# Kernel tuning notes

Measured on AMD Instinct MI355X. Metric: run time of the kernel, lower is better.

## Reference

```python
import jax, jax.numpy as jnp
import numpy as np

N, P, C, S, H, CLS = 32, 16, 256, 128, 4, 3000
DH = C // H
EPS = 1e-5


def setup_inputs() -> dict:
    key = jax.random.key(0)
    ks = jax.random.split(key, 8)
    sh = (N, P, C, S)
    return {
        "t_f": jax.random.normal(ks[0], sh, jnp.float32),
        "t_s": jax.random.normal(ks[1], sh, jnp.float32),
        "t_l": jax.random.normal(ks[2], sh, jnp.float32),
        # grouped 1x1 conv weights, one [out_ch, in_ch] matrix per part
        "decay_w": jax.random.normal(ks[3], (P, C, 3 * C), jnp.float32) * 0.02,
        "qkv_w": jax.random.normal(ks[4], (P, 3 * C, C), jnp.float32) * 0.02,
        "out_w": jax.random.normal(ks[5], (P, C, C), jnp.float32) * 0.02,
        # per-part BatchNorm1d affine params
        "gamma": jnp.ones((P, C), jnp.float32),
        "beta": jnp.zeros((P, C), jnp.float32),
        # classifier fc: [in_planes, class_num] (broadcast over parts)
        "fc": jax.random.normal(ks[6], (C, CLS), jnp.float32) * 0.02,
    }


def reference(t_f, t_s, t_l, decay_w, qkv_w, out_w, gamma, beta, fc):
    n, p, c, s = t_f.shape
    h, dh = H, DH
    scale = dh ** -0.5

    # decay_c: grouped 1x1 conv, 3c -> c per part
    x_cat = jnp.concatenate([t_f, t_s, t_l], axis=2)            # [n,p,3c,s]
    t_all = jnp.einsum('npis,poi->npos', x_cat, decay_w)        # [n,p,c,s]

    # Attention.to_qkv: grouped 1x1 conv, c -> 3c per part
    qkv = jnp.einsum('npcs,pqc->npqs', t_all, qkv_w)            # [n,p,3c,s]
    qkv = qkv.reshape(n, p, 3, h, dh, s).transpose(2, 0, 3, 1, 4, 5)  # [3,n,h,p,dh,s]
    q, k, v = qkv[0], qkv[1], qkv[2]

    # frame-frame attention per (head, part): [n,h,p,s,s]
    dots = jnp.einsum('nhpcs,nhpct->nhpst', q, k) * scale
    attn = jax.nn.softmax(dots, axis=-1)

    o = jnp.einsum('nhpst,nhpct->nhpcs', attn, v)               # [n,h,p,dh,s]
    o = o.transpose(0, 2, 1, 3, 4).reshape(n, p, c, s)          # [n,p,c,s]
    o = jnp.einsum('npcs,poc->npos', o, out_w)                  # to_out grouped conv

    # residual + max over frames
    wpv = (o + t_all).max(axis=-1)                              # [n,p,c]

    # select_topk_part (topk_num == 1 forced by squeeze(2) in torch code):
    # argmax over frames of column-summed attention, gather that frame of t_f, sum heads
    idx = jnp.argmax(attn.sum(axis=-2), axis=-1)                # [n,h,p]
    ib = jnp.broadcast_to(idx[:, :, :, None, None], (n, h, p, c, 1))
    sel = jnp.take_along_axis(t_f[:, None], ib, axis=-1)[..., 0]  # [n,h,p,c]
    sel = sel.sum(axis=1)                                       # [n,p,c]

    # per-part BatchNorm1d in training mode (batch statistics over n)
    mean = wpv.mean(axis=0)                                     # [p,c]
    var = wpv.var(axis=0)                                       # biased, as torch BN
    pf = (wpv - mean) / jnp.sqrt(var + EPS) * gamma + beta      # [n,p,c]

    cls = jnp.einsum('npc,ck->npk', pf, fc)                     # [n,p,class_num]
    return cls, wpv.transpose(1, 0, 2), sel.transpose(1, 0, 2)
```

## Files before the change

### kernel.cpp

```cpp
#include <hip/hip_runtime.h>
#include <math.h>

#define N_ 32
#define P_ 16
#define C_ 256
#define S_ 128
#define H_ 4
#define CLS_ 3000

typedef __attribute__((ext_vector_type(4))) float f4v;
typedef __attribute__((ext_vector_type(4))) float f32x4;
typedef __attribute__((ext_vector_type(8))) short short8;
typedef __attribute__((ext_vector_type(4))) unsigned short us4;

__device__ __forceinline__ unsigned short f2bf(float x){
    unsigned u = __float_as_uint(x);
    u += 0x7fffu + ((u >> 16) & 1u);
    return (unsigned short)(u >> 16);
}
__device__ __forceinline__ float bf2f(unsigned short h){
    return __uint_as_float(((unsigned)h) << 16);
}

typedef __attribute__((address_space(1))) const unsigned int gu32_t;
typedef __attribute__((address_space(3))) unsigned int lu32_t;
__device__ __forceinline__ void gload16(const void* g, void* l){
    __builtin_amdgcn_global_load_lds((gu32_t*)g, (lu32_t*)l, 16, 0, 0);
}

__global__ void wsplit(const float* __restrict__ dw, const float* __restrict__ qw,
                       const float* __restrict__ ow,
                       unsigned short* __restrict__ wdh, unsigned short* __restrict__ wdl,
                       unsigned short* __restrict__ wqh, unsigned short* __restrict__ wql,
                       unsigned short* __restrict__ woh){
    int i = blockIdx.x * 256 + threadIdx.x;
    int stride = gridDim.x * 256;
    for (; i < 3145728; i += stride){
        float a = dw[i]; unsigned short h = f2bf(a);
        wdh[i] = h; wdl[i] = f2bf(a - bf2f(h));
        float b = qw[i]; unsigned short h2 = f2bf(b);
        wqh[i] = h2; wql[i] = f2bf(b - bf2f(h2));
        if (i < 1048576) woh[i] = f2bf(ow[i]);
    }
}

__global__ __launch_bounds__(256) void fct_kernel(const float* __restrict__ fc,
                                                  unsigned short* __restrict__ fcT){
    int n = blockIdx.x * 256 + threadIdx.x;
    if (n < CLS_){
        for (int c = 0; c < 256; ++c) fcT[(size_t)n * 256 + c] = f2bf(fc[(size_t)c * CLS_ + n]);
    } else {
        for (int c = 0; c < 256; ++c) fcT[(size_t)n * 256 + c] = 0;
    }
}

__global__ __launch_bounds__(256) void gemm0t(
    const float* __restrict__ t_f, const float* __restrict__ t_s,
    const float* __restrict__ t_l,
    const unsigned short* __restrict__ Whi, const unsigned short* __restrict__ Wlo,
    unsigned short* __restrict__ outH, unsigned short* __restrict__ outL,
    int n0, int cnp)
{
    __shared__ unsigned short sm[24576];
    float* Tf = (float*)sm;
    unsigned short* AhL = sm + 8192;
    unsigned short* AlL = sm + 12288;
    unsigned short* BhL = sm + 16384;
    unsigned short* BlL = sm + 20480;
    unsigned short* Ep  = sm;

    const int id = blockIdx.x;
    const int xcd = id & 7;
    const int r = id >> 3;
    const int ppl = r / (cnp * 2);
    const int rr = r % (cnp * 2);
    const int n_l = rr >> 1;
    const int o_t = rr & 1;
    const int p = xcd * 2 + ppl;
    const int np_l = n_l * 16 + p;
    const int o0 = o_t * 128;
    const size_t np_g = (size_t)(n0 + n_l) * 16 + p;

    const int tid = threadIdx.x;
    const int w = tid >> 6, l = tid & 63;
    const int lr = l & 15, lg = l >> 4;
    const int ws0 = (w & 1) * 64, wo0 = (w >> 1) * 64;
    const int s2 = tid & 127, khalf = tid >> 7;

    const unsigned short* Wp_h = Whi + ((size_t)p * 256 + o0) * 768;
    const unsigned short* Wp_l = Wlo + ((size_t)p * 256 + o0) * 768;

    f32x4 acc[4][4];
#pragma unroll
    for (int i = 0; i < 4; ++i)
#pragma unroll
        for (int j = 0; j < 4; ++j) acc[i][j] = (f32x4){0.f, 0.f, 0.f, 0.f};

    for (int k0 = 0; k0 < 768; k0 += 32){
        const int t = k0 >> 8;
        const float* src = (t == 0) ? t_f : ((t == 1) ? t_s : t_l);
        const float* xbase = src + (np_g * 256 + (k0 & 255)) * 128;
#pragma unroll
        for (int it = 0; it < 4; ++it){
            int lin = (w * 4 + it) * 64 + l;
            gload16(xbase + lin * 4, Tf + lin * 4);
        }
#pragma unroll
        for (int it = 0; it < 2; ++it){
            int lin = (w * 2 + it) * 64 + l;
            int row = lin >> 2, ch = lin & 3;
            int sk = ((ch ^ ((row >> 1) & 3)) << 3);
            gload16(Wp_h + (size_t)row * 768 + k0 + sk, BhL + lin * 8);
            gload16(Wp_l + (size_t)row * 768 + k0 + sk, BlL + lin * 8);
        }
        __syncthreads();
        {
            short8 h0, h1, l0, l1;
#pragma unroll
            for (int j = 0; j < 8; ++j){
                float v = Tf[(khalf * 16 + j) * 128 + s2];
                unsigned short hh = f2bf(v);
                h0[j] = (short)hh; l0[j] = (short)f2bf(v - bf2f(hh));
            }
#pragma unroll
            for (int j = 0; j < 8; ++j){
                float v = Tf[(khalf * 16 + 8 + j) * 128 + s2];
                unsigned short hh = f2bf(v);
                h1[j] = (short)hh; l1[j] = (short)f2bf(v - bf2f(hh));
            }
            int sb = (s2 >> 1) & 3;
            int c0 = (khalf * 2) ^ sb, c1 = (khalf * 2 + 1) ^ sb;
            *(short8*)(AhL + s2 * 32 + c0 * 8) = h0;
            *(short8*)(AhL + s2 * 32 + c1 * 8) = h1;
            *(short8*)(AlL + s2 * 32 + c0 * 8) = l0;
            *(short8*)(AlL + s2 * 32 + c1 * 8) = l1;
        }
        __syncthreads();
        short8 ah[4], al[4];
#pragma unroll
        for (int sf = 0; sf < 4; ++sf){
            int row = ws0 + sf * 16 + lr;
            int cof = (lg ^ ((row >> 1) & 3)) << 3;
            ah[sf] = *(const short8*)(AhL + row * 32 + cof);
            al[sf] = *(const short8*)(AlL + row * 32 + cof);
        }
#pragma unroll
        for (int of = 0; of < 4; ++of){
            int row = wo0 + of * 16 + lr;
            int cof = (lg ^ ((row >> 1) & 3)) << 3;
            short8 bh = *(const short8*)(BhL + row * 32 + cof);
            short8 bl = *(const short8*)(BlL + row * 32 + cof);
#pragma unroll
            for (int sf = 0; sf < 4; ++sf){
                acc[sf][of] = __builtin_amdgcn_mfma_f32_16x16x32_bf16(ah[sf], bh, acc[sf][of], 0, 0, 0);
                acc[sf][of] = __builtin_amdgcn_mfma_f32_16x16x32_bf16(ah[sf], bl, acc[sf][of], 0, 0, 0);
                acc[sf][of] = __builtin_amdgcn_mfma_f32_16x16x32_bf16(al[sf], bh, acc[sf][of], 0, 0, 0);
            }
        }
        __syncthreads();
    }

#pragma unroll
    for (int plane = 0; plane < 2; ++plane){
#pragma unroll
        for (int sf = 0; sf < 4; ++sf)
#pragma unroll
            for (int of = 0; of < 4; ++of){
                int col = wo0 + of * 16 + lr;
#pragma unroll
                for (int r2 = 0; r2 < 4; ++r2){
                    int row = ws0 + sf * 16 + lg * 4 + r2;
                    float v = acc[sf][of][r2];
                    unsigned short hh = f2bf(v);
                    unsigned short q = plane ? f2bf(v - bf2f(hh)) : hh;
                    Ep[row * 136 + col] = q;
                }
            }
        __syncthreads();
        unsigned short* dst = plane ? outL : outH;
#pragma unroll
        for (int it = 0; it < 8; ++it){
            int idx = tid + 256 * it;
            int row = idx >> 4, seg = (idx & 15) * 8;
            *(short8*)(dst + (size_t)np_l * 128 * 256 + (size_t)row * 256 + o0 + seg) =
                *(const short8*)(Ep + row * 136 + seg);
        }
        __syncthreads();
    }
}

template<int KEXT, int APITCH, int ND, int MODE, int OPITCH, int TOB>
__global__ __launch_bounds__(256) void gemm3(
    const unsigned short* __restrict__ Ah_g, const unsigned short* __restrict__ Al_g,
    const unsigned short* __restrict__ Whi, const unsigned short* __restrict__ Wlo,
    const unsigned short* __restrict__ resH, const unsigned short* __restrict__ resL,
    unsigned short* __restrict__ outH, unsigned short* __restrict__ outL,
    float* __restrict__ outF, int n0, int cnp)
{
    constexpr int T3 = (MODE == 2) ? 0 : 1;
    constexpr int OB = ND / TOB;
    constexpr int OF = TOB / 32;
    __shared__ unsigned short sm[T3 ? 17408 : (4096 + TOB * 32)];
    unsigned short* AhL = sm;
    unsigned short* BhL = sm + 4096;
    unsigned short* AlL = T3 ? (sm + 8192) : sm;
    unsigned short* BlL = T3 ? (sm + 12288) : sm;
    unsigned short* Ep = sm;
    __shared__ float cmax[2][2][64];

    const int id = blockIdx.x;
    const int xcd = id & 7;
    const int r = id >> 3;
    const int ppl = r / (cnp * OB);
    const int rr = r % (cnp * OB);
    const int n_l = rr / OB;
    const int o_t = rr % OB;
    const int p = xcd * 2 + ppl;
    const int np_l = n_l * 16 + p;
    const int o0 = o_t * TOB;

    const int tid = threadIdx.x;
    const int w = tid >> 6, l = tid & 63;
    const int lr = l & 15, lg = l >> 4;
    const int ws0 = (w & 1) * 64, wo0 = (w >> 1) * (TOB / 2);
    const size_t aBase = (size_t)np_l * 128 * APITCH;
    const unsigned short* Wp_h = Whi + ((size_t)p * ND + o0) * KEXT;
    const unsigned short* Wp_l = T3 ? (Wlo + ((size_t)p * ND + o0) * KEXT) : Wp_h;

    f32x4 acc[4][OF];
#pragma unroll
    for (int i = 0; i < 4; ++i)
#pragma unroll
        for (int j = 0; j < OF; ++j) acc[i][j] = (f32x4){0.f, 0.f, 0.f, 0.f};

    for (int k0 = 0; k0 < KEXT; k0 += 32){
#pragma unroll
        for (int it = 0; it < 2; ++it){
            int slot = w * 2 + it;
            int lin = slot * 64 + l;
            int row = lin >> 2, ch = lin & 3;
            int sk = ((ch ^ ((row >> 1) & 3)) << 3);
            gload16(Ah_g + aBase + (size_t)row * APITCH + k0 + sk, AhL + slot * 512);
            if (T3)
                gload16(Al_g + aBase + (size_t)row * APITCH + k0 + sk, AlL + slot * 512);
        }
#pragma unroll
        for (int it = 0; it < TOB / 64; ++it){
            int slot = w * (TOB / 64) + it;
            int lin = slot * 64 + l;
            int row = lin >> 2, ch = lin & 3;
            int sk = ((ch ^ ((row >> 1) & 3)) << 3);
            gload16(Wp_h + (size_t)row * KEXT + k0 + sk, BhL + slot * 512);
            if (T3)
                gload16(Wp_l + (size_t)row * KEXT + k0 + sk, BlL + slot * 512);
        }
        __syncthreads();
        short8 ah[4], al[4];
#pragma unroll
        for (int sf = 0; sf < 4; ++sf){
            int row = ws0 + sf * 16 + lr;
            int cof = (lg ^ ((row >> 1) & 3)) << 3;
            ah[sf] = *(const short8*)(AhL + row * 32 + cof);
            if (T3) al[sf] = *(const short8*)(AlL + row * 32 + cof);
        }
#pragma unroll
        for (int of = 0; of < OF; ++of){
            int row = wo0 + of * 16 + lr;
            int cof = (lg ^ ((row >> 1) & 3)) << 3;
            short8 bh = *(const short8*)(BhL + row * 32 + cof);
            short8 bl = bh;
            if (T3) bl = *(const short8*)(BlL + row * 32 + cof);
#pragma unroll
            for (int sf = 0; sf < 4; ++sf){
                acc[sf][of] = __builtin_amdgcn_mfma_f32_16x16x32_bf16(ah[sf], bh, acc[sf][of], 0, 0, 0);
                if (T3){
                    acc[sf][of] = __builtin_amdgcn_mfma_f32_16x16x32_bf16(ah[sf], bl, acc[sf][of], 0, 0, 0);
                    acc[sf][of] = __builtin_amdgcn_mfma_f32_16x16x32_bf16(al[sf], bh, acc[sf][of], 0, 0, 0);
                }
            }
        }
        __syncthreads();
    }

    if (MODE != 2){
#pragma unroll
        for (int plane = 0; plane < 2; ++plane){
#pragma unroll
            for (int sf = 0; sf < 4; ++sf)
#pragma unroll
                for (int of = 0; of < OF; ++of){
                    int col = wo0 + of * 16 + lr;
#pragma unroll
                    for (int r2 = 0; r2 < 4; ++r2){
                        int row = ws0 + sf * 16 + lg * 4 + r2;
                        float v = acc[sf][of][r2];
                        unsigned short hh = f2bf(v);
                        unsigned short q = plane ? f2bf(v - bf2f(hh)) : hh;
                        Ep[row * 136 + col] = q;
                    }
                }
            __syncthreads();
            unsigned short* dst = plane ? outL : outH;
#pragma unroll
            for (int it = 0; it < 8; ++it){
                int idx = tid + 256 * it;
                int row = idx >> 4, seg = (idx & 15) * 8;
                *(short8*)(dst + (size_t)np_l * 128 * OPITCH + (size_t)row * OPITCH + o0 + seg) =
                    *(const short8*)(Ep + row * 136 + seg);
            }
            __syncthreads();
        }
    } else {
        const int n_g = n0 + n_l;
#pragma unroll
        for (int of = 0; of < OF; ++of){
            int oc = o0 + wo0 + of * 16 + lr;
            float m = -INFINITY;
#pragma unroll
            for (int sf = 0; sf < 4; ++sf){
#pragma unroll
                for (int r2 = 0; r2 < 4; ++r2){
                    int s = ws0 + sf * 16 + lg * 4 + r2;
                    size_t ri = (size_t)np_l * 128 * 256 + (size_t)s * 256 + oc;
                    float v = acc[sf][of][r2] + bf2f(resH[ri]) + bf2f(resL[ri]);
                    m = fmaxf(m, v);
                }
            }
            m = fmaxf(m, __shfl_xor(m, 16));
            m = fmaxf(m, __shfl_xor(m, 32));
            if (l < 16) cmax[w >> 1][w & 1][of * 16 + l] = m;
        }
        __syncthreads();
        if (tid < TOB){
            int oh = tid >> 5, col = tid & 31;
            float v = fmaxf(cmax[oh][0][col], cmax[oh][1][col]);
            outF[((size_t)p * N_ + n_g) * C_ + o0 + oh * 32 + col] = v;
        }
    }
}

__global__ __launch_bounds__(256) void attn3(unsigned short* __restrict__ qH,
                                             const unsigned short* __restrict__ qL,
                                             int* __restrict__ idxA, int n0, int cnp){
    __shared__ char smraw[17408 + 34816 + 2048];
    unsigned short* Vs = (unsigned short*)smraw;
    unsigned short* Pm = (unsigned short*)(smraw + 17408);
    float* csW = (float*)(smraw + 17408 + 34816);
    unsigned short* Ot = (unsigned short*)smraw;

    const int id = blockIdx.x;
    const int xcd = id & 7;
    const int r = id >> 3;
    const int ppl = r / (cnp * 4);
    const int rr = r % (cnp * 4);
    const int n_l = rr >> 2, h = rr & 3;
    const int p = xcd * 2 + ppl;
    const int np_l = n_l * 16 + p;
    const int tid = threadIdx.x, w = tid >> 6, l = tid & 63;
    const int lr = l & 15, lg = l >> 4;
    unsigned short* baseH = qH + (size_t)np_l * 128 * 768;
    const unsigned short* baseL = qL + (size_t)np_l * 128 * 768;

#pragma unroll
    for (int it = 0; it < 8; ++it){
        int idx = tid + 256 * it;
        int t = idx >> 4, d4 = (idx & 15) * 4;
        us4 v = *(const us4*)(baseH + (size_t)t * 768 + 512 + h * 64 + d4);
#pragma unroll
        for (int j = 0; j < 4; ++j) Vs[(d4 + j) * 136 + t] = v[j];
    }

    short8 qh[2][2], ql[2][2];
#pragma unroll
    for (int sf = 0; sf < 2; ++sf)
#pragma unroll
        for (int ks = 0; ks < 2; ++ks){
            size_t off = (size_t)(w * 32 + sf * 16 + lr) * 768 + h * 64 + ks * 32 + lg * 8;
            qh[sf][ks] = *(const short8*)(baseH + off);
            ql[sf][ks] = *(const short8*)(baseL + off);
        }

    f32x4 dacc[2][8];
#pragma unroll
    for (int i = 0; i < 2; ++i)
#pragma unroll
        for (int j = 0; j < 8; ++j) dacc[i][j] = (f32x4){0.f, 0.f, 0.f, 0.f};

#pragma unroll
    for (int tf = 0; tf < 8; ++tf){
#pragma unroll
        for (int ks = 0; ks < 2; ++ks){
            size_t off = (size_t)(tf * 16 + lr) * 768 + 256 + h * 64 + ks * 32 + lg * 8;
            short8 kh = *(const short8*)(baseH + off);
            short8 kl = *(const short8*)(baseL + off);
#pragma unroll
            for (int sf = 0; sf < 2; ++sf){
                dacc[sf][tf] = __builtin_amdgcn_mfma_f32_16x16x32_bf16(qh[sf][ks], kh, dacc[sf][tf], 0, 0, 0);
                dacc[sf][tf] = __builtin_amdgcn_mfma_f32_16x16x32_bf16(qh[sf][ks], kl, dacc[sf][tf], 0, 0, 0);
                dacc[sf][tf] = __builtin_amdgcn_mfma_f32_16x16x32_bf16(ql[sf][ks], kh, dacc[sf][tf], 0, 0, 0);
            }
        }
    }

    float csp[8];
#pragma unroll
    for (int tf = 0; tf < 8; ++tf) csp[tf] = 0.f;
#pragma unroll
    for (int sf = 0; sf < 2; ++sf){
#pragma unroll
        for (int r2 = 0; r2 < 4; ++r2){
            float m = -INFINITY;
#pragma unroll
            for (int tf = 0; tf < 8; ++tf) m = fmaxf(m, dacc[sf][tf][r2]);
            m = fmaxf(m, __shfl_xor(m, 1)); m = fmaxf(m, __shfl_xor(m, 2));
            m = fmaxf(m, __shfl_xor(m, 4)); m = fmaxf(m, __shfl_xor(m, 8));
            float e[8]; float sum = 0.f;
#pragma unroll
            for (int tf = 0; tf < 8; ++tf){
                e[tf] = __expf(0.125f * (dacc[sf][tf][r2] - m)); sum += e[tf];
            }
            sum += __shfl_xor(sum, 1); sum += __shfl_xor(sum, 2);
            sum += __shfl_xor(sum, 4); sum += __shfl_xor(sum, 8);
            float inv = 1.f / sum;
            int s = w * 32 + sf * 16 + lg * 4 + r2;
#pragma unroll
            for (int tf = 0; tf < 8; ++tf){
                float pv = e[tf] * inv;
                Pm[s * 136 + tf * 16 + lr] = f2bf(pv);
                csp[tf] += pv;
            }
        }
    }
#pragma unroll
    for (int tf = 0; tf < 8; ++tf){
        float v = csp[tf];
        v += __shfl_xor(v, 16); v += __shfl_xor(v, 32);
        if (l < 16) csW[w * 128 + tf * 16 + l] = v;
    }
    __syncthreads();

    f32x4 oacc[8];
#pragma unroll
    for (int i = 0; i < 8; ++i) oacc[i] = (f32x4){0.f, 0.f, 0.f, 0.f};
#pragma unroll
    for (int ks = 0; ks < 4; ++ks){
        short8 av = *(const short8*)(Vs + (w * 16 + lr) * 136 + ks * 32 + lg * 8);
#pragma unroll
        for (int sf = 0; sf < 8; ++sf){
            short8 bp = *(const short8*)(Pm + (sf * 16 + lr) * 136 + ks * 32 + lg * 8);
            oacc[sf] = __builtin_amdgcn_mfma_f32_16x16x32_bf16(av, bp, oacc[sf], 0, 0, 0);
        }
    }
    __syncthreads();

    if (tid < 64){
        float v0 = csW[tid] + csW[128 + tid] + csW[256 + tid] + csW[384 + tid];
        float v1 = csW[64 + tid] + csW[192 + tid] + csW[320 + tid] + csW[448 + tid];
        float bv; int bi;
        if (v1 > v0){ bv = v1; bi = 64 + tid; } else { bv = v0; bi = tid; }
#pragma unroll
        for (int msk = 1; msk <= 32; msk <<= 1){
            float ov = __shfl_xor(bv, msk); int oi = __shfl_xor(bi, msk);
            if (ov > bv || (ov == bv && oi < bi)){ bv = ov; bi = oi; }
        }
        if (tid == 0){ int n_g = n0 + n_l; idxA[(n_g * H_ + h) * P_ + p] = bi; }
    }

#pragma unroll
    for (int sf = 0; sf < 8; ++sf){
        int s = sf * 16 + lr;
#pragma unroll
        for (int r2 = 0; r2 < 4; ++r2) Ot[s * 72 + w * 16 + lg * 4 + r2] = f2bf(oacc[sf][r2]);
    }
    __syncthreads();
#pragma unroll
    for (int it = 0; it < 4; ++it){
        int idx = tid + 256 * it;
        int s = idx >> 3, d8 = (idx & 7) * 8;
        *(short8*)(baseH + (size_t)s * 768 + h * 64 + d8) = *(const short8*)(Ot + s * 72 + d8);
    }
}

__global__ void bn_stats(const float* __restrict__ wpvT,
                         const float* __restrict__ gamma,
                         const float* __restrict__ beta,
                         float* __restrict__ aArr, float* __restrict__ bArr)
{
    int i = blockIdx.x * blockDim.x + threadIdx.x;
    if (i >= P_ * C_) return;
    int p = i / C_, c = i % C_;
    const float* basep = wpvT + (size_t)p * N_ * C_ + c;
    float su = 0.f, s2 = 0.f;
    for (int n = 0; n < N_; ++n){
        float v = basep[n * C_];
        su += v; s2 += v * v;
    }
    float mean = su * (1.f / N_);
    float var = s2 * (1.f / N_) - mean * mean;
    float rstd = rsqrtf(var + 1e-5f);
    float a = gamma[i] * rstd;
    aArr[i] = a;
    bArr[i] = beta[i] - mean * a;
}

__global__ __launch_bounds__(256) void pf_kernel(const float* __restrict__ wpvT,
                                                 const float* __restrict__ aArr,
                                                 const float* __restrict__ bArr,
                                                 unsigned short* __restrict__ pfb){
    int m = blockIdx.x, c = threadIdx.x;
    int p = m >> 5;
    float v = wpvT[(size_t)m * 256 + c];
    pfb[(size_t)m * 256 + c] = f2bf(v * aArr[p * 256 + c] + bArr[p * 256 + c]);
}

__global__ __launch_bounds__(256) void gemmc(const unsigned short* __restrict__ pfb,
                                             const unsigned short* __restrict__ fcT,
                                             float* __restrict__ cls){
    __shared__ unsigned short sm[2 * 128 * 72];
    unsigned short* AhL = sm;
    unsigned short* BhL = sm + 128 * 72;

    const int tid = threadIdx.x;
    const int w = tid >> 6, l = tid & 63;
    const int lr = l & 15, lg = l >> 4;
    const int ws0 = (w & 1) * 64, wo0 = (w >> 1) * 64;
    const int o0 = blockIdx.x * 128;
    const int m0 = blockIdx.y * 128;

    f32x4 acc[4][4];
#pragma unroll
    for (int i = 0; i < 4; ++i)
#pragma unroll
        for (int j = 0; j < 4; ++j) acc[i][j] = (f32x4){0.f, 0.f, 0.f, 0.f};

    for (int k0 = 0; k0 < 256; k0 += 64){
#pragma unroll
        for (int it = 0; it < 4; ++it){
            int idx = tid + 256 * it;
            int s = idx >> 3, c8 = (idx & 7) * 8;
            *(short8*)(AhL + s * 72 + c8) = *(const short8*)(pfb + (size_t)(m0 + s) * 256 + k0 + c8);
            *(short8*)(BhL + s * 72 + c8) = *(const short8*)(fcT + (size_t)(o0 + s) * 256 + k0 + c8);
        }
        __syncthreads();
#pragma unroll
        for (int ks = 0; ks < 2; ++ks){
            short8 ah[4];
#pragma unroll
            for (int sf = 0; sf < 4; ++sf)
                ah[sf] = *(const short8*)(AhL + (ws0 + sf * 16 + lr) * 72 + ks * 32 + lg * 8);
#pragma unroll
            for (int of = 0; of < 4; ++of){
                short8 bh = *(const short8*)(BhL + (wo0 + of * 16 + lr) * 72 + ks * 32 + lg * 8);
#pragma unroll
                for (int sf = 0; sf < 4; ++sf)
                    acc[sf][of] = __builtin_amdgcn_mfma_f32_16x16x32_bf16(ah[sf], bh, acc[sf][of], 0, 0, 0);
            }
        }
        __syncthreads();
    }
#pragma unroll
    for (int sf = 0; sf < 4; ++sf)
#pragma unroll
        for (int of = 0; of < 4; ++of){
            int oc = o0 + wo0 + of * 16 + lr;
            if (oc < CLS_){
#pragma unroll
                for (int r2 = 0; r2 < 4; ++r2){
                    int m = m0 + ws0 + sf * 16 + lg * 4 + r2;
                    int n = m & 31, p = m >> 5;
                    cls[((size_t)n * 16 + p) * CLS_ + oc] = acc[sf][of][r2];
                }
            }
        }
}

__global__ void sel_kernel(const float* __restrict__ t_f,
                           const int* __restrict__ idxArr,
                           float* __restrict__ selT)
{
    const int np = blockIdx.x;
    const int n = np >> 4, p = np & 15;
    const int c = threadIdx.x;
    float acc = 0.f;
#pragma unroll
    for (int h = 0; h < H_; ++h){
        int s = idxArr[(n * H_ + h) * P_ + p];
        acc += t_f[((size_t)np * C_ + c) * S_ + s];
    }
    selT[((size_t)p * N_ + n) * C_ + c] = acc;
}

extern "C" void kernel_launch(void* const* d_in, const int* in_sizes, int n_in,
                              void* d_out, int out_size, void* d_ws, size_t ws_size,
                              hipStream_t stream)
{
    const float* t_f     = (const float*)d_in[0];
    const float* t_s     = (const float*)d_in[1];
    const float* t_l     = (const float*)d_in[2];
    const float* decay_w = (const float*)d_in[3];
    const float* qkv_w   = (const float*)d_in[4];
    const float* out_w   = (const float*)d_in[5];
    const float* gamma   = (const float*)d_in[6];
    const float* beta    = (const float*)d_in[7];
    const float* fc      = (const float*)d_in[8];
    float* out = (float*)d_out;

    const size_t WD = 3145728, WQ = 3145728, WO = 1048576;
    char* basep = (char*)d_ws;
    unsigned short* wdh = (unsigned short*)basep;
    unsigned short* wdl = wdh + WD;
    unsigned short* wqh = wdl + WD;
    unsigned short* wql = wqh + WQ;
    unsigned short* woh = wql + WQ;
    unsigned short* fcT = woh + WO;
    unsigned short* pfb = fcT + 3072 * 256;
    float* aArr = (float*)(pfb + 512 * 256);
    float* bArr = aArr + P_ * C_;
    int* idxA = (int*)(bArr + P_ * C_);
    char* big = (char*)(idxA + N_ * H_ * P_);
    size_t head = (size_t)(big - basep);
    size_t avail = (ws_size > head) ? (ws_size - head) : 0;
    const size_t per_n = (size_t)16 * 128 * (256 + 768) * 2 * 2;
    int cn = (int)(avail / per_n);
    if (cn < 1) cn = 1;
    if (cn > N_) cn = N_;
    int nch = (N_ + cn - 1) / cn;
    cn = (N_ + nch - 1) / nch;

    unsigned short* tH = (unsigned short*)big;
    unsigned short* tL = tH + (size_t)cn * 16 * 128 * 256;
    unsigned short* qH = tL + (size_t)cn * 16 * 128 * 256;
    unsigned short* qL = qH + (size_t)cn * 16 * 128 * 768;

    float* cls  = out;
    float* wpvT = out + (size_t)N_ * P_ * CLS_;
    float* selT = wpvT + (size_t)P_ * N_ * C_;

    wsplit<<<2048, 256, 0, stream>>>(decay_w, qkv_w, out_w, wdh, wdl, wqh, wql, woh);
    fct_kernel<<<12, 256, 0, stream>>>(fc, fcT);

    for (int n0 = 0; n0 < N_; n0 += cn){
        int c = (N_ - n0 < cn) ? (N_ - n0) : cn;
        int npg = c * 16;
        gemm0t<<<npg * 2, 256, 0, stream>>>(
            t_f, t_s, t_l, wdh, wdl, tH, tL, n0, c);
        gemm3<256, 256, 768, 1, 768, 128><<<npg * 6, 256, 0, stream>>>(
            tH, tL, wqh, wql, nullptr, nullptr, qH, qL, nullptr, n0, c);
        attn3<<<c * 64, 256, 0, stream>>>(qH, qL, idxA, n0, c);
        gemm3<256, 768, 256, 2, 256, 64><<<npg * 4, 256, 0, stream>>>(
            qH, qH, woh, woh, tH, tL, nullptr, nullptr, wpvT, n0, c);
    }
    bn_stats<<<(P_ * C_ + 255) / 256, 256, 0, stream>>>(wpvT, gamma, beta, aArr, bArr);
    pf_kernel<<<512, 256, 0, stream>>>(wpvT, aArr, bArr, pfb);
    gemmc<<<dim3(24, 4), 256, 0, stream>>>(pfb, fcT, cls);
    sel_kernel<<<N_ * P_, 256, 0, stream>>>(t_f, idxA, selT);
}
```

Baseline: 443.7 us.

## Pair two batch samples per QKV GEMM block to reuse weight tiles

Adds a specialized QKV projection kernel in which each block computes a 128-wide output slice for two batch samples of the same part. Each loaded weight tile is therefore shared across 256 rows instead of 128, which halves weight traffic per output and raises MFMA work per LDS load. Block IDs are mapped so that parts are grouped by XCD, aiming for L2 locality of the per-part weights. The trade-off is more accumulator registers (4x8 tiles per wave), a larger LDS footprint that may lower occupancy, a two-pass epilogue, and half as many blocks in the grid.

```diff
diff --git a/kernel.cpp b/kernel.cpp
--- a/kernel.cpp
+++ b/kernel.cpp
@@ -186,6 +186,127 @@
                 *(const short8*)(Ep + row * 136 + seg);
         }
         __syncthreads();
+    }
+}
+
+__global__ __launch_bounds__(256) void gemm3b(
+    const unsigned short* __restrict__ Ah_g, const unsigned short* __restrict__ Al_g,
+    const unsigned short* __restrict__ Whi, const unsigned short* __restrict__ Wlo,
+    unsigned short* __restrict__ outH, unsigned short* __restrict__ outL,
+    int cnp, int npair)
+{
+    __shared__ unsigned short sm[24576];
+    unsigned short* A1h = sm;
+    unsigned short* A1l = sm + 4096;
+    unsigned short* A2h = sm + 8192;
+    unsigned short* A2l = sm + 12288;
+    unsigned short* BhL = sm + 16384;
+    unsigned short* BlL = sm + 20480;
+    unsigned short* Ep  = sm;
+
+    const int id = blockIdx.x;
+    const int xcd = id & 7;
+    const int r = id >> 3;
+    const int per_ppl = npair * 6;
+    const int ppl = r / per_ppl;
+    const int rr = r % per_ppl;
+    const int pi = rr / 6;
+    const int o_t = rr % 6;
+    const int p = xcd * 2 + ppl;
+    const int n1 = 2 * pi;
+    const int n2 = (2 * pi + 1 < cnp) ? (2 * pi + 1) : (2 * pi);
+    const int npl1 = n1 * 16 + p;
+    const int npl2 = n2 * 16 + p;
+    const int o0 = o_t * 128;
+
+    const int tid = threadIdx.x;
+    const int w = tid >> 6, l = tid & 63;
+    const int lr = l & 15, lg = l >> 4;
+    const size_t aB1 = (size_t)npl1 * 128 * 256;
+    const size_t aB2 = (size_t)npl2 * 128 * 256;
+    const unsigned short* Wp_h = Whi + ((size_t)p * 768 + o0) * 256;
+    const unsigned short* Wp_l = Wlo + ((size_t)p * 768 + o0) * 256;
+
+    f32x4 acc[4][8];
+#pragma unroll
+    for (int i = 0; i < 4; ++i)
+#pragma unroll
+        for (int j = 0; j < 8; ++j) acc[i][j] = (f32x4){0.f, 0.f, 0.f, 0.f};
+
+    for (int k0 = 0; k0 < 256; k0 += 32){
+#pragma unroll
+        for (int it = 0; it < 2; ++it){
+            int slot = w * 2 + it;
+            int lin = slot * 64 + l;
+            int row = lin >> 2, ch = lin & 3;
+            int sk = ((ch ^ ((row >> 1) & 3)) << 3);
+            size_t ro = (size_t)row * 256 + k0 + sk;
+            gload16(Ah_g + aB1 + ro, A1h + slot * 512);
+            gload16(Al_g + aB1 + ro, A1l + slot * 512);
+            gload16(Ah_g + aB2 + ro, A2h + slot * 512);
+            gload16(Al_g + aB2 + ro, A2l + slot * 512);
+            gload16(Wp_h + ro, BhL + slot * 512);
+            gload16(Wp_l + ro, BlL + slot * 512);
+        }
+        __syncthreads();
+        const unsigned short* Awh = (w < 2) ? A1h : A2h;
+        const unsigned short* Awl = (w < 2) ? A1l : A2l;
+        short8 ah[4], al[4];
+#pragma unroll
+        for (int sf = 0; sf < 4; ++sf){
+            int row = (w & 1) * 64 + sf * 16 + lr;
+            int cof = (lg ^ ((row >> 1) & 3)) << 3;
+            ah[sf] = *(const short8*)(Awh + row * 32 + cof);
+            al[sf] = *(const short8*)(Awl + row * 32 + cof);
+        }
+#pragma unroll
+        for (int of = 0; of < 8; ++of){
+            int brow = of * 16 + lr;
+            int bcof = (lg ^ ((brow >> 1) & 3)) << 3;
+            short8 bh = *(const short8*)(BhL + brow * 32 + bcof);
+            short8 bl = *(const short8*)(BlL + brow * 32 + bcof);
+#pragma unroll
+            for (int sf = 0; sf < 4; ++sf){
+                acc[sf][of] = __builtin_amdgcn_mfma_f32_16x16x32_bf16(ah[sf], bh, acc[sf][of], 0, 0, 0);
+                acc[sf][of] = __builtin_amdgcn_mfma_f32_16x16x32_bf16(ah[sf], bl, acc[sf][of], 0, 0, 0);
+                acc[sf][of] = __builtin_amdgcn_mfma_f32_16x16x32_bf16(al[sf], bh, acc[sf][of], 0, 0, 0);
+            }
+        }
+        __syncthreads();
+    }
+
+#pragma unroll
+    for (int plane = 0; plane < 2; ++plane){
+#pragma unroll
+        for (int half = 0; half < 2; ++half){
+            if ((w >> 1) == half){
+#pragma unroll
+                for (int sf = 0; sf < 4; ++sf)
+#pragma unroll
+                    for (int of = 0; of < 8; ++of){
+                        int col = of * 16 + lr;
+#pragma unroll
+                        for (int r2 = 0; r2 < 4; ++r2){
+                            int row = (w & 1) * 64 + sf * 16 + lg * 4 + r2;
+                            float v = acc[sf][of][r2];
+                            unsigned short hh = f2bf(v);
+                            unsigned short q = plane ? f2bf(v - bf2f(hh)) : hh;
+                            Ep[row * 136 + col] = q;
+                        }
+                    }
+            }
+            __syncthreads();
+            unsigned short* dst = (plane ? outL : outH) +
+                (size_t)(half ? npl2 : npl1) * 128 * 768;
+#pragma unroll
+            for (int it = 0; it < 8; ++it){
+                int idx = tid + 256 * it;
+                int row = idx >> 4, seg = (idx & 15) * 8;
+                *(short8*)(dst + (size_t)row * 768 + o0 + seg) =
+                    *(const short8*)(Ep + row * 136 + seg);
+            }
+            __syncthreads();
+        }
     }
 }
 
@@ -642,10 +763,11 @@
     for (int n0 = 0; n0 < N_; n0 += cn){
         int c = (N_ - n0 < cn) ? (N_ - n0) : cn;
         int npg = c * 16;
+        int npair = (c + 1) >> 1;
         gemm0t<<<npg * 2, 256, 0, stream>>>(
             t_f, t_s, t_l, wdh, wdl, tH, tL, n0, c);
-        gemm3<256, 256, 768, 1, 768, 128><<<npg * 6, 256, 0, stream>>>(
-            tH, tL, wqh, wql, nullptr, nullptr, qH, qL, nullptr, n0, c);
+        gemm3b<<<npair * 96, 256, 0, stream>>>(
+            tH, tL, wqh, wql, qH, qL, c, npair);
         attn3<<<c * 64, 256, 0, stream>>>(qH, qL, idxA, n0, c);
         gemm3<256, 768, 256, 2, 256, 64><<<npg * 4, 256, 0, stream>>>(
             qH, qH, woh, woh, tH, tL, nullptr, nullptr, wpvT, n0, c);
```

Result: slower. 489.8 us (+10.4%).
